# Performance work log

Measured on AMD Instinct MI355X. Metric: run time of the kernel, lower is better.

Reference implementation:

```python
import jax, jax.numpy as jnp
import numpy as np

N = 50000   # nodes
F = 32      # num_node_features
EMB = 32    # embedding_size
R = 8       # num_relations
L = 5       # num_layers
E = 400000  # edges


def setup_inputs() -> dict:
    key = jax.random.key(0)
    ks = jax.random.split(key, 12)
    s = 0.1  # weight scale ~ 1/sqrt(fan_in) for stability over 5 residual layers
    return {
        "x": jax.random.normal(ks[0], (N, F), jnp.float32),
        "edge_index": jax.random.randint(ks[1], (2, E), 0, N, jnp.int32),
        "edge_type": jax.random.randint(ks[2], (E,), 0, R, jnp.int32),
        "edge_dist": jax.random.uniform(ks[3], (E,), jnp.float32),
        "fc_W": jax.random.normal(ks[4], (F, EMB), jnp.float32) * s,
        "fc_b": jnp.zeros((EMB,), jnp.float32),
        "rgcn_W": jax.random.normal(ks[5], (L, R, EMB, EMB), jnp.float32) * s,
        "rgcn_root": jax.random.normal(ks[6], (L, EMB, EMB), jnp.float32) * s,
        "rgcn_bias": jnp.zeros((L, EMB), jnp.float32),
        "mlp_W1": jax.random.normal(ks[7], (1 + R, EMB), jnp.float32) * s,
        "mlp_b1": jnp.zeros((EMB,), jnp.float32),
        "mlp_W2": jax.random.normal(ks[8], (EMB, EMB * EMB), jnp.float32) * s,
        "mlp_b2": jnp.zeros((EMB * EMB,), jnp.float32),
        "nn_root": jax.random.normal(ks[9], (L, EMB, EMB), jnp.float32) * s,
        "nn_bias": jnp.zeros((L, EMB), jnp.float32),
    }


def _forward(x, edge_index, edge_type, edge_dist, fc_W, fc_b, rgcn_W, rgcn_root,
             rgcn_bias, mlp_W1, mlp_b1, mlp_W2, mlp_b2, nn_root, nn_bias):
    n = x.shape[0]
    src, dst = edge_index[0], edge_index[1]  # source_to_target flow

    # edge_attr_c = [distance, onehot(edge_type)] : [E, 1+R]
    onehot = jax.nn.one_hot(edge_type, R, dtype=x.dtype)
    eattr = jnp.concatenate([edge_dist[:, None], onehot], axis=1)

    # Shared edge_mlp -> per-edge [EMB, EMB] weight (same for every NNConv layer)
    We = (jax.nn.relu(eattr @ mlp_W1 + mlp_b1) @ mlp_W2 + mlp_b2).reshape(-1, EMB, EMB)

    # degree for NNConv mean aggregation
    deg = jax.ops.segment_sum(jnp.ones_like(edge_dist), dst, num_segments=n)
    denom = jnp.maximum(deg, 1.0)[:, None]

    # per-relation in-degree for RGCN per-relation mean
    rel_cnt = []
    for r in range(R):
        c = jax.ops.segment_sum((edge_type == r).astype(x.dtype), dst, num_segments=n)
        rel_cnt.append(jnp.maximum(c, 1.0)[:, None])

    h = jax.nn.relu(x @ fc_W + fc_b)
    for l in range(L):
        # RGCNConv: root transform + per-relation mean of W_r x_j
        out = h @ rgcn_root[l] + rgcn_bias[l]
        for r in range(R):
            mask_r = (edge_type == r).astype(h.dtype)[:, None]
            msg = (h @ rgcn_W[l, r])[src] * mask_r  # [E, EMB]
            out = out + jax.ops.segment_sum(msg, dst, num_segments=n) / rel_cnt[r]
        h_disc = jax.nn.relu(out)

        # NNConv: x_j @ Theta(e) per edge, mean-aggregated, + root + bias
        msg = jnp.einsum('ei,eio->eo', h[src], We)  # [E, EMB]
        agg = jax.ops.segment_sum(msg, dst, num_segments=n) / denom
        h_cont = jax.nn.relu(h @ nn_root[l] + agg + nn_bias[l])

        h = h + h_disc + h_cont
    return h


def reference(x, edge_index, edge_type, edge_dist, fc_W, fc_b, rgcn_W, rgcn_root,
              rgcn_bias, mlp_W1, mlp_b1, mlp_W2, mlp_b2, nn_root, nn_bias):
    return _forward(x, edge_index, edge_type, edge_dist, fc_W, fc_b, rgcn_W,
                    rgcn_root, rgcn_bias, mlp_W1, mlp_b1, mlp_W2, mlp_b2,
                    nn_root, nn_bias)
```

## Files before the change

### kernel.cpp

```cpp
#include <hip/hip_runtime.h>

#define N_NODES 50000
#define N_EDGES 400000
#define EMB 32
#define NREL 8
#define NLAYER 5
#define NPB 16
#define NBLK (N_NODES / NPB)
#define KROWS 43
#define NCHUNK 196
#define E2CAP (N_EDGES + 8 * N_NODES)

typedef __attribute__((ext_vector_type(8))) short short8;
typedef __attribute__((ext_vector_type(4))) float f32x4;
typedef __attribute__((ext_vector_type(4))) unsigned int u32x4v;

__device__ __forceinline__ unsigned short f2bf(float f) {
    unsigned u = __float_as_uint(f);
    unsigned r = u + 0x7FFF + ((u >> 16) & 1);
    return (unsigned short)(r >> 16);
}

__device__ __forceinline__ unsigned cvt_pk(float a, float b) {
    unsigned r;
    asm("v_cvt_pk_bf16_f32 %0, %1, %2" : "=v"(r) : "v"(a), "v"(b));
    return r;
}


__global__ __launch_bounds__(256) void fill_kernel(int* __restrict__ zeroblk,
                                                   int2* __restrict__ edge2,
                                                   float* __restrict__ ha,
                                                   float* __restrict__ hb) {
    int i = blockIdx.x * 256 + threadIdx.x;
    if (i < E2CAP) edge2[i] = make_int2(N_NODES, 0);
    if (i < 10 * N_NODES) zeroblk[i] = 0;
    if (i < EMB) { ha[(size_t)N_NODES * EMB + i] = 0.0f; hb[(size_t)N_NODES * EMB + i] = 0.0f; }
}

__global__ __launch_bounds__(256) void hist_kernel(const int* __restrict__ ei,
                                                   const int* __restrict__ et,
                                                   int* __restrict__ deg,
                                                   int* __restrict__ relcnt) {
    int e = blockIdx.x * 256 + threadIdx.x;
    if (e < N_EDGES) {
        int d = ei[N_EDGES + e];
        atomicAdd(&deg[d], 1);
        atomicAdd(&relcnt[d * NREL + et[e]], 1);
    }
}

__device__ __forceinline__ int pdeg_of(int d) {
    return (d > 0 ? d + 7 : 8) & ~7;
}

__global__ __launch_bounds__(256) void nodeprep_kernel(const int* __restrict__ deg,
                                                       const int* __restrict__ relcnt,
                                                       int* __restrict__ bsum,
                                                       float* __restrict__ invdeg,
                                                       float* __restrict__ invcnt,
                                                       unsigned char* __restrict__ perm) {
    __shared__ int wsum[4];
    int tid = threadIdx.x, lane = tid & 63, wv = tid >> 6;
    int i = blockIdx.x * 256 + tid;
    int d = (i < N_NODES) ? deg[i] : 0;
    int v = (i < N_NODES) ? pdeg_of(d) : 0;
    #pragma unroll
    for (int off = 32; off > 0; off >>= 1) v += __shfl_down(v, off, 64);
    if (lane == 0) wsum[wv] = v;
    __syncthreads();
    if (tid == 0) bsum[blockIdx.x] = wsum[0] + wsum[1] + wsum[2] + wsum[3];
    if (i < N_NODES) {
        invdeg[i] = 1.0f / (float)(d > 0 ? d : 1);
        #pragma unroll
        for (int r = 0; r < NREL; r++) {
            int c = relcnt[i * NREL + r];
            invcnt[i * NREL + r] = 1.0f / (float)(c > 0 ? c : 1);
        }
    }
    if (i < NBLK) {
        int dd[NPB]; unsigned char idx[NPB];
        #pragma unroll
        for (int k = 0; k < NPB; k++) { dd[k] = deg[i * NPB + k]; idx[k] = (unsigned char)k; }
        for (int a = 1; a < NPB; a++) {
            int dv = dd[a]; unsigned char iv = idx[a];
            int j = a - 1;
            while (j >= 0 && dd[j] < dv) { dd[j + 1] = dd[j]; idx[j + 1] = idx[j]; j--; }
            dd[j + 1] = dv; idx[j + 1] = iv;
        }
        #pragma unroll
        for (int k = 0; k < NPB; k++) perm[i * NPB + k] = idx[k];
    }
}

__global__ __launch_bounds__(256) void boff_kernel(const int* __restrict__ bsum,
                                                   int* __restrict__ boff,
                                                   int* __restrict__ row_ptr) {
    __shared__ int ws[4];
    int tid = threadIdx.x, lane = tid & 63, w = tid >> 6;
    int v = (tid < NCHUNK) ? bsum[tid] : 0;
    int incl = v;
    #pragma unroll
    for (int off = 1; off < 64; off <<= 1) {
        int t = __shfl_up(incl, off, 64);
        if (lane >= off) incl += t;
    }
    if (lane == 63) ws[w] = incl;
    __syncthreads();
    int add = 0;
    for (int j = 0; j < w; j++) add += ws[j];
    if (tid < NCHUNK) boff[tid] = add + incl - v;
    if (tid == 0) row_ptr[N_NODES] = ws[0] + ws[1] + ws[2] + ws[3];
}

__global__ __launch_bounds__(256) void rptr_kernel(const int* __restrict__ deg,
                                                   const int* __restrict__ boff,
                                                   int* __restrict__ row_ptr) {
    __shared__ int ws[4];
    int tid = threadIdx.x, lane = tid & 63, w = tid >> 6;
    int i = blockIdx.x * 256 + tid;
    int v = (i < N_NODES) ? pdeg_of(deg[i]) : 0;
    int incl = v;
    #pragma unroll
    for (int off = 1; off < 64; off <<= 1) {
        int t = __shfl_up(incl, off, 64);
        if (lane >= off) incl += t;
    }
    if (lane == 63) ws[w] = incl;
    __syncthreads();
    int add = boff[blockIdx.x];
    for (int j = 0; j < w; j++) add += ws[j];
    if (i < N_NODES) row_ptr[i] = add + incl - v;
}

__global__ __launch_bounds__(256) void scatter_kernel(const int* __restrict__ ei,
                                                      const int* __restrict__ et,
                                                      const float* __restrict__ ed,
                                                      const int* __restrict__ row_ptr,
                                                      int* __restrict__ cursor,
                                                      int2* __restrict__ edge2,
                                                      const unsigned char* __restrict__ perm,
                                                      int4* __restrict__ wavetab) {
    int e = blockIdx.x * 256 + threadIdx.x;
    if (e < N_EDGES) {
        int d = ei[N_EDGES + e];
        int pos = row_ptr[d] + atomicAdd(&cursor[d], 1);
        edge2[pos] = make_int2(ei[e] | (et[e] << 16), __float_as_int(ed[e]));
    }
    if (e < NBLK * 8) {
        int b = e >> 3, wv = e & 7;
        int s0 = perm[b * NPB + wv], s1 = perm[b * NPB + (NPB - 1 - wv)];
        int nA = b * NPB + s0, nB = b * NPB + s1;
        int pb0 = row_ptr[nA], pd0 = row_ptr[nA + 1] - pb0;
        int pb1 = row_ptr[nB], pd1 = row_ptr[nB + 1] - pb1;
        wavetab[e] = make_int4(s0 | (s1 << 8), pb0, pb1, pd0 | (pd1 << 16));
    }
}

__global__ __launch_bounds__(256) void wtbf_kernel(const float* __restrict__ W2,
                                                   const float* __restrict__ b2,
                                                   const float* __restrict__ rgcnW,
                                                   const float* __restrict__ rgcnRoot,
                                                   const float* __restrict__ nnRoot,
                                                   unsigned short* __restrict__ WB) {
    int m = blockIdx.x;
    const float* src;
    if (m < 32) src = W2 + (size_t)m * 1024;
    else if (m == 32) src = b2;
    else {
        int t = m - 33, l = t / 10, j = t % 10;
        src = (j < 8) ? rgcnW + (size_t)(l * 8 + j) * 1024
            : (j == 8) ? rgcnRoot + (size_t)l * 1024
                       : nnRoot + (size_t)l * 1024;
    }
    unsigned short* dst = WB + (size_t)m * 1024;
    #pragma unroll
    for (int c = 0; c < 4; c++) {
        int idx = c * 256 + threadIdx.x;
        int o = idx >> 5, k = idx & 31;
        int i = (k >> 1) + ((k & 1) << 4);
        dst[o * 32 + k] = f2bf(src[i * 32 + o]);
    }
}


__global__ __launch_bounds__(256) void fc_kernel(const float* __restrict__ x,
                                                 const float* __restrict__ W,
                                                 const float* __restrict__ b,
                                                 float* __restrict__ h) {
    __shared__ __align__(16) float xt[8][EMB];
    int tid = threadIdx.x;
    int nl = tid >> 5, lane = tid & 31;
    int n0 = blockIdx.x * 8;
    xt[tid >> 5][tid & 31] = x[n0 * EMB + tid];
    __syncthreads();
    float acc = b[lane];
    #pragma unroll
    for (int i = 0; i < EMB; i++) acc += xt[nl][i] * W[i * EMB + lane];
    int ol = ((lane & 15) << 1) | (lane >> 4);
    h[(n0 + nl) * EMB + ol] = fmaxf(acc, 0.0f);
}


__device__ __forceinline__ void gath(const float* __restrict__ h, int4 E, int m,
                                     float2& ga, float2& gb) {
    ga = *(const float2*)&h[((E.x & 0xFFFF) << 5) + 2 * m];
    gb = *(const float2*)&h[((E.z & 0xFFFF) << 5) + 2 * m];
}

__device__ __forceinline__ void proc_pair(int4 E, float2 ga, float2 gb,
                                          const float2* wrb2f, float w10_0, float w10_1,
                                          unsigned selm, int m,
                                          unsigned& A0s, unsigned& A1s, unsigned& ASs,
                                          unsigned& B0s, unsigned& B1s) {
    int ra = (E.x >> 16) & 7, rb = (E.z >> 16) & 7;
    float2 wa = wrb2f[ra * 16 + m];
    float2 wb = wrb2f[rb * 16 + m];
    float da = __int_as_float(E.y), db = __int_as_float(E.w);
    float hA0 = fmaxf(fmaf(da, w10_0, wa.x), 0.f);
    float hA1 = fmaxf(fmaf(da, w10_1, wa.y), 0.f);
    float hB0 = fmaxf(fmaf(db, w10_0, wb.x), 0.f);
    float hB1 = fmaxf(fmaf(db, w10_1, wb.y), 0.f);
    A0s = cvt_pk(hA0, hB0);
    A1s = cvt_pk(hA1, hB1);
    ASs = cvt_pk((float)((selm >> ra) & 1u), (float)((selm >> rb) & 1u));
    B0s = cvt_pk(ga.x, gb.x);
    B1s = cvt_pk(ga.y, gb.y);
}

__device__ __forceinline__ void mfma6(const unsigned* fa0v, const unsigned* fa1v,
                                      const unsigned* fasv, const unsigned* fb0v,
                                      const unsigned* fb1v,
                                      f32x4& aP00, f32x4& aP01, f32x4& aP10, f32x4& aP11,
                                      f32x4& aS0, f32x4& aS1) {
    u32x4v u0 = {fa0v[0], fa0v[1], fa0v[2], fa0v[3]};
    u32x4v u1 = {fa1v[0], fa1v[1], fa1v[2], fa1v[3]};
    u32x4v us = {fasv[0], fasv[1], fasv[2], fasv[3]};
    u32x4v v0 = {fb0v[0], fb0v[1], fb0v[2], fb0v[3]};
    u32x4v v1 = {fb1v[0], fb1v[1], fb1v[2], fb1v[3]};
    short8 A0 = __builtin_bit_cast(short8, u0);
    short8 A1 = __builtin_bit_cast(short8, u1);
    short8 AS = __builtin_bit_cast(short8, us);
    short8 B0 = __builtin_bit_cast(short8, v0);
    short8 B1 = __builtin_bit_cast(short8, v1);
    aP00 = __builtin_amdgcn_mfma_f32_16x16x32_bf16(A0, B0, aP00, 0, 0, 0);
    aP01 = __builtin_amdgcn_mfma_f32_16x16x32_bf16(A0, B1, aP01, 0, 0, 0);
    aP10 = __builtin_amdgcn_mfma_f32_16x16x32_bf16(A1, B0, aP10, 0, 0, 0);
    aP11 = __builtin_amdgcn_mfma_f32_16x16x32_bf16(A1, B1, aP11, 0, 0, 0);
    aS0  = __builtin_amdgcn_mfma_f32_16x16x32_bf16(AS, B0, aS0, 0, 0, 0);
    aS1  = __builtin_amdgcn_mfma_f32_16x16x32_bf16(AS, B1, aS1, 0, 0, 0);
}

__device__ __forceinline__ void edge_pass(const float* __restrict__ h,
                                          const int2* __restrict__ edge2,
                                          const float2* wrb2f,
                                          int pb, int pe, int quad, int m,
                                          float w10_0, float w10_1, unsigned selm,
                                          int4 E0, float2 g0a, float2 g0b,
                                          f32x4& aP00, f32x4& aP01, f32x4& aP10,
                                          f32x4& aP11, f32x4& aS0, f32x4& aS1) {
    {
        unsigned fa0v[4] = {0,0,0,0}, fa1v[4] = {0,0,0,0}, fasv[4] = {0,0,0,0};
        unsigned fb0v[4] = {0,0,0,0}, fb1v[4] = {0,0,0,0};
        proc_pair(E0, g0a, g0b, wrb2f, w10_0, w10_1, selm, m,
                  fa0v[0], fa1v[0], fasv[0], fb0v[0], fb1v[0]);
        if (pb + 8 < pe) {
            int4 E = *(const int4*)&edge2[pb + 8 + quad * 2];
            float2 ga, gb; gath(h, E, m, ga, gb);
            proc_pair(E, ga, gb, wrb2f, w10_0, w10_1, selm, m,
                      fa0v[1], fa1v[1], fasv[1], fb0v[1], fb1v[1]);
        }
        if (pb + 16 < pe) {
            int4 E = *(const int4*)&edge2[pb + 16 + quad * 2];
            float2 ga, gb; gath(h, E, m, ga, gb);
            proc_pair(E, ga, gb, wrb2f, w10_0, w10_1, selm, m,
                      fa0v[2], fa1v[2], fasv[2], fb0v[2], fb1v[2]);
        }
        if (pb + 24 < pe) {
            int4 E = *(const int4*)&edge2[pb + 24 + quad * 2];
            float2 ga, gb; gath(h, E, m, ga, gb);
            proc_pair(E, ga, gb, wrb2f, w10_0, w10_1, selm, m,
                      fa0v[3], fa1v[3], fasv[3], fb0v[3], fb1v[3]);
        }
        mfma6(fa0v, fa1v, fasv, fb0v, fb1v, aP00, aP01, aP10, aP11, aS0, aS1);
    }
    for (int c0 = pb + 32; c0 < pe; c0 += 32) {
        unsigned fa0v[4] = {0,0,0,0}, fa1v[4] = {0,0,0,0}, fasv[4] = {0,0,0,0};
        unsigned fb0v[4] = {0,0,0,0}, fb1v[4] = {0,0,0,0};
        {
            int4 E = *(const int4*)&edge2[c0 + quad * 2];
            float2 ga, gb; gath(h, E, m, ga, gb);
            proc_pair(E, ga, gb, wrb2f, w10_0, w10_1, selm, m,
                      fa0v[0], fa1v[0], fasv[0], fb0v[0], fb1v[0]);
        }
        if (c0 + 8 < pe) {
            int4 E = *(const int4*)&edge2[c0 + 8 + quad * 2];
            float2 ga, gb; gath(h, E, m, ga, gb);
            proc_pair(E, ga, gb, wrb2f, w10_0, w10_1, selm, m,
                      fa0v[1], fa1v[1], fasv[1], fb0v[1], fb1v[1]);
        }
        if (c0 + 16 < pe) {
            int4 E = *(const int4*)&edge2[c0 + 16 + quad * 2];
            float2 ga, gb; gath(h, E, m, ga, gb);
            proc_pair(E, ga, gb, wrb2f, w10_0, w10_1, selm, m,
                      fa0v[2], fa1v[2], fasv[2], fb0v[2], fb1v[2]);
        }
        if (c0 + 24 < pe) {
            int4 E = *(const int4*)&edge2[c0 + 24 + quad * 2];
            float2 ga, gb; gath(h, E, m, ga, gb);
            proc_pair(E, ga, gb, wrb2f, w10_0, w10_1, selm, m,
                      fa0v[3], fa1v[3], fasv[3], fb0v[3], fb1v[3]);
        }
        mfma6(fa0v, fa1v, fasv, fb0v, fb1v, aP00, aP01, aP10, aP11, aS0, aS1);
    }
}

__device__ __forceinline__ void stage_node(unsigned short (*P)[EMB], int quad, int m,
                                           float idg, const float* __restrict__ invcnt_n,
                                           const float* __restrict__ hrow,
                                           const f32x4& aP00, const f32x4& aP01,
                                           const f32x4& aP10, const f32x4& aP11,
                                           const f32x4& aS0, const f32x4& aS1) {
    #pragma unroll
    for (int reg = 0; reg < 4; ++reg) {
        const int row = quad * 4 + reg;
        *(unsigned*)&P[row][2 * m]      = cvt_pk(aP00[reg] * idg, aP01[reg] * idg);
        *(unsigned*)&P[row + 16][2 * m] = cvt_pk(aP10[reg] * idg, aP11[reg] * idg);
        if (row <= 8) {
            const float sc = (row == 0) ? idg : invcnt_n[row - 1];
            *(unsigned*)&P[32 + row][2 * m] = cvt_pk(aS0[reg] * sc, aS1[reg] * sc);
        }
    }
    if (quad < 2) {
        float2 hh = *(const float2*)&hrow[2 * m];
        *(unsigned*)&P[41 + quad][2 * m] = cvt_pk(hh.x, hh.y);
    }
}

__global__ __launch_bounds__(512, 6) void layer_kernel(
    const float* __restrict__ h,
    const int2* __restrict__ edge2,
    const int4* __restrict__ wavetab,
    const float* __restrict__ invdeg,
    const float* __restrict__ invcnt,
    const float* __restrict__ W1,
    const float* __restrict__ b1,
    const unsigned short* __restrict__ WBs,
    const unsigned short* __restrict__ WBl,
    const float* __restrict__ rgcnBias_l,
    const float* __restrict__ nnBias_l,
    float* __restrict__ hout,
    int last)
{
    __shared__ __align__(16) unsigned short P_lds[NPB][KROWS][EMB];
    __shared__ __align__(16) float2 wrb2f[NREL * 16];

    const int tid = threadIdx.x;
    const int n0 = blockIdx.x * NPB;

    if (tid < 128) {
        int r = tid >> 4, mi = tid & 15;
        wrb2f[r * 16 + mi] = make_float2(W1[(1 + r) * EMB + mi] + b1[mi],
                                         W1[(1 + r) * EMB + mi + 16] + b1[mi + 16]);
    }

    const int l    = tid & 63;
    const int w    = tid >> 6;
    const int quad = l >> 4;
    const int m    = l & 15;
    const float w10_0 = W1[m];
    const float w10_1 = W1[m + 16];
    const unsigned selm = (m == 0) ? 0xFFu : (m <= 8 ? (1u << (m - 1)) : 0u);

    int4 wt = wavetab[blockIdx.x * 8 + w];
    const int hw0 = wt.x & 0xFF, hw1 = (wt.x >> 8) & 0xFF;
    const int pb0 = wt.y, pe0 = wt.y + (wt.w & 0xFFFF);
    const int pb1 = wt.z, pe1 = wt.z + (int)((unsigned)wt.w >> 16);
    int4 E0 = *(const int4*)&edge2[pb0 + quad * 2];
    int4 E1 = *(const int4*)&edge2[pb1 + quad * 2];
    float2 g0a, g0b, g1a, g1b;
    gath(h, E0, m, g0a, g0b);
    gath(h, E1, m, g1a, g1b);

    __syncthreads();

    {
        f32x4 aP00 = {0,0,0,0}, aP01 = {0,0,0,0}, aP10 = {0,0,0,0}, aP11 = {0,0,0,0};
        f32x4 aS0 = {0,0,0,0}, aS1 = {0,0,0,0};
        edge_pass(h, edge2, wrb2f, pb0, pe0, quad, m, w10_0, w10_1, selm,
                  E0, g0a, g0b, aP00, aP01, aP10, aP11, aS0, aS1);
        const int n = n0 + hw0;
        stage_node(P_lds[hw0], quad, m, invdeg[n], invcnt + (size_t)n * NREL,
                   h + (size_t)n * EMB, aP00, aP01, aP10, aP11, aS0, aS1);
    }
    {
        f32x4 aP00 = {0,0,0,0}, aP01 = {0,0,0,0}, aP10 = {0,0,0,0}, aP11 = {0,0,0,0};
        f32x4 aS0 = {0,0,0,0}, aS1 = {0,0,0,0};
        edge_pass(h, edge2, wrb2f, pb1, pe1, quad, m, w10_0, w10_1, selm,
                  E1, g1a, g1b, aP00, aP01, aP10, aP11, aS0, aS1);
        const int n = n0 + hw1;
        stage_node(P_lds[hw1], quad, m, invdeg[n], invcnt + (size_t)n * NREL,
                   h + (size_t)n * EMB, aP00, aP01, aP10, aP11, aS0, aS1);
    }
    __syncthreads();

    const int node16 = l & 15;
    const int o0 = l & 15;

    f32x4 accN0 = {0,0,0,0}, accN1 = {0,0,0,0};
    f32x4 accR0 = {0,0,0,0}, accR1 = {0,0,0,0};

    #pragma unroll
    for (int j = 0; j < 6; j++) {
        const int rr = w + 8 * j;
        if (rr < KROWS) {
            const unsigned short* Bsrc = (rr < 33) ? (WBs + (size_t)rr * 1024)
                                                   : (WBl + (size_t)(rr - 33) * 1024);
            short8 bf0 = *(const short8*)(Bsrc + o0 * 32 + quad * 8);
            short8 bf1 = *(const short8*)(Bsrc + (o0 + 16) * 32 + quad * 8);
            short8 a = *(const short8*)&P_lds[node16][rr][quad * 8];
            if (rr <= 32 || rr == 42) {
                accN0 = __builtin_amdgcn_mfma_f32_16x16x32_bf16(a, bf0, accN0, 0, 0, 0);
                accN1 = __builtin_amdgcn_mfma_f32_16x16x32_bf16(a, bf1, accN1, 0, 0, 0);
            } else {
                accR0 = __builtin_amdgcn_mfma_f32_16x16x32_bf16(a, bf0, accR0, 0, 0, 0);
                accR1 = __builtin_amdgcn_mfma_f32_16x16x32_bf16(a, bf1, accR1, 0, 0, 0);
            }
        }
    }
    __syncthreads();

    float* RedAll = (float*)&P_lds[0][0][0];
    {
        float* my = RedAll + w * 1024;
        #pragma unroll
        for (int reg = 0; reg < 4; reg++) {
            int nd = quad * 4 + reg;
            my[nd * 32 + o0]            = accN0[reg];
            my[nd * 32 + o0 + 16]       = accN1[reg];
            my[512 + nd * 32 + o0]      = accR0[reg];
            my[512 + nd * 32 + o0 + 16] = accR1[reg];
        }
    }
    __syncthreads();

    {
        const int hw2 = tid >> 5, lane = tid & 31;
        const int n2 = n0 + hw2;
        float sn = 0.0f, sr = 0.0f;
        #pragma unroll
        for (int ww = 0; ww < 8; ww++) {
            sn += RedAll[ww * 1024 + tid];
            sr += RedAll[ww * 1024 + 512 + tid];
        }
        const int il = ((lane & 15) << 1) | (lane >> 4);
        float hd = h[(size_t)n2 * EMB + il];
        float o_r = fmaxf(sr + rgcnBias_l[lane], 0.0f);
        float o_n = fmaxf(sn + nnBias_l[lane], 0.0f);
        hout[(size_t)n2 * EMB + (last ? lane : il)] = hd + o_r + o_n;
    }
}


extern "C" void kernel_launch(void* const* d_in, const int* in_sizes, int n_in,
                              void* d_out, int out_size, void* d_ws, size_t ws_size,
                              hipStream_t stream) {
    const float* x        = (const float*)d_in[0];
    const int*   ei       = (const int*)d_in[1];
    const int*   et       = (const int*)d_in[2];
    const float* ed       = (const float*)d_in[3];
    const float* fcW      = (const float*)d_in[4];
    const float* fcb      = (const float*)d_in[5];
    const float* rgcnW    = (const float*)d_in[6];
    const float* rgcnRoot = (const float*)d_in[7];
    const float* rgcnBias = (const float*)d_in[8];
    const float* W1       = (const float*)d_in[9];
    const float* b1       = (const float*)d_in[10];
    const float* W2       = (const float*)d_in[11];
    const float* b2       = (const float*)d_in[12];
    const float* nnRoot   = (const float*)d_in[13];
    const float* nnBias   = (const float*)d_in[14];

    float* ws = (float*)d_ws;
    float* h_a    = ws;  ws += (size_t)(N_NODES + 1) * EMB;
    float* h_b    = ws;  ws += (size_t)(N_NODES + 1) * EMB;
    float* invdeg = ws;  ws += (size_t)N_NODES;
    float* invcnt = ws;  ws += (size_t)N_NODES * NREL;
    unsigned short* WB = (unsigned short*)ws;  ws += (size_t)83 * 1024 / 2;
    int2* edge2   = (int2*)ws;     ws += (size_t)E2CAP * 2;
    int* row_ptr  = (int*)ws;      ws += (size_t)(N_NODES + 1);
    int* bsum     = (int*)ws;      ws += (size_t)NCHUNK;
    int* boff     = (int*)ws;      ws += (size_t)NCHUNK;
    int* deg      = (int*)ws;      ws += (size_t)N_NODES;
    int* relcnt   = (int*)ws;      ws += (size_t)N_NODES * NREL;
    int* cursor   = (int*)ws;      ws += (size_t)N_NODES;
    unsigned char* perm = (unsigned char*)ws;  ws += (size_t)NBLK * NPB / 4;
    int4* wavetab = (int4*)ws;     ws += (size_t)NBLK * 8 * 4;
    (void)in_sizes; (void)n_in; (void)out_size; (void)ws_size;

    fill_kernel<<<(E2CAP + 255) / 256, 256, 0, stream>>>(deg, edge2, h_a, h_b);
    hist_kernel<<<(N_EDGES + 255) / 256, 256, 0, stream>>>(ei, et, deg, relcnt);
    nodeprep_kernel<<<NCHUNK, 256, 0, stream>>>(deg, relcnt, bsum, invdeg, invcnt, perm);
    boff_kernel<<<1, 256, 0, stream>>>(bsum, boff, row_ptr);
    rptr_kernel<<<NCHUNK, 256, 0, stream>>>(deg, boff, row_ptr);
    scatter_kernel<<<(N_EDGES + 255) / 256, 256, 0, stream>>>(ei, et, ed, row_ptr,
                                                              cursor, edge2, perm, wavetab);
    wtbf_kernel<<<83, 256, 0, stream>>>(W2, b2, rgcnW, rgcnRoot, nnRoot, WB);
    fc_kernel<<<N_NODES / 8, 256, 0, stream>>>(x, fcW, fcb, h_a);

    const float* hin = h_a;
    float* houtb = h_b;
    for (int l = 0; l < NLAYER; l++) {
        float* dst = (l == NLAYER - 1) ? (float*)d_out : houtb;
        layer_kernel<<<NBLK, 512, 0, stream>>>(
            hin, edge2, wavetab, invdeg, invcnt, W1, b1,
            WB, WB + (size_t)(33 + l * 10) * 1024,
            rgcnBias + (size_t)l * EMB,
            nnBias + (size_t)l * EMB,
            dst, (l == NLAYER - 1) ? 1 : 0);
        float* old_in = (float*)hin;
        hin = dst;
        houtb = old_in;
    }
}
```

Baseline: 395.8 us.

## Schedule nodes globally by padded degree bucket, one node per wave

Replaces the per-block sort of 16 consecutive nodes with a global counting sort of nodes into padded-degree buckets. Each 1024-thread block now handles 16 nodes of similar degree, one node per wave, so waves inside a block stay balanced. The output reduction becomes two-phase across 16 waves, and the edge-list padding is written only into the padding slots inside scatter instead of a full prefill. The trade-offs are global atomics on 32 bucket counters, scattered node access per block that loses locality, and larger blocks that may lower occupancy.

```diff
diff --git a/kernel.cpp b/kernel.cpp
--- a/kernel.cpp
+++ b/kernel.cpp
@@ -27,14 +27,16 @@
     return r;
 }
 
+__device__ __forceinline__ int pdeg_of(int d) {
+    return (d > 0 ? d + 7 : 8) & ~7;
+}
+
 
 __global__ __launch_bounds__(256) void fill_kernel(int* __restrict__ zeroblk,
-                                                   int2* __restrict__ edge2,
                                                    float* __restrict__ ha,
                                                    float* __restrict__ hb) {
     int i = blockIdx.x * 256 + threadIdx.x;
-    if (i < E2CAP) edge2[i] = make_int2(N_NODES, 0);
-    if (i < 10 * N_NODES) zeroblk[i] = 0;
+    if (i < 10 * N_NODES + 64) zeroblk[i] = 0;
     if (i < EMB) { ha[(size_t)N_NODES * EMB + i] = 0.0f; hb[(size_t)N_NODES * EMB + i] = 0.0f; }
 }
 
@@ -50,16 +52,12 @@
     }
 }
 
-__device__ __forceinline__ int pdeg_of(int d) {
-    return (d > 0 ? d + 7 : 8) & ~7;
-}
-
 __global__ __launch_bounds__(256) void nodeprep_kernel(const int* __restrict__ deg,
                                                        const int* __restrict__ relcnt,
                                                        int* __restrict__ bsum,
                                                        float* __restrict__ invdeg,
                                                        float* __restrict__ invcnt,
-                                                       unsigned char* __restrict__ perm) {
+                                                       int* __restrict__ bcnt) {
     __shared__ int wsum[4];
     int tid = threadIdx.x, lane = tid & 63, wv = tid >> 6;
     int i = blockIdx.x * 256 + tid;
@@ -77,25 +75,16 @@
             int c = relcnt[i * NREL + r];
             invcnt[i * NREL + r] = 1.0f / (float)(c > 0 ? c : 1);
         }
-    }
-    if (i < NBLK) {
-        int dd[NPB]; unsigned char idx[NPB];
-        #pragma unroll
-        for (int k = 0; k < NPB; k++) { dd[k] = deg[i * NPB + k]; idx[k] = (unsigned char)k; }
-        for (int a = 1; a < NPB; a++) {
-            int dv = dd[a]; unsigned char iv = idx[a];
-            int j = a - 1;
-            while (j >= 0 && dd[j] < dv) { dd[j + 1] = dd[j]; idx[j + 1] = idx[j]; j--; }
-            dd[j + 1] = dv; idx[j + 1] = iv;
-        }
-        #pragma unroll
-        for (int k = 0; k < NPB; k++) perm[i * NPB + k] = idx[k];
+        int bkt = pdeg_of(d) >> 3; bkt = (bkt > 32 ? 32 : bkt) - 1;
+        atomicAdd(&bcnt[bkt], 1);
     }
 }
 
 __global__ __launch_bounds__(256) void boff_kernel(const int* __restrict__ bsum,
                                                    int* __restrict__ boff,
-                                                   int* __restrict__ row_ptr) {
+                                                   int* __restrict__ row_ptr,
+                                                   const int* __restrict__ bcnt,
+                                                   int* __restrict__ bcur) {
     __shared__ int ws[4];
     int tid = threadIdx.x, lane = tid & 63, w = tid >> 6;
     int v = (tid < NCHUNK) ? bsum[tid] : 0;
@@ -110,16 +99,23 @@
     int add = 0;
     for (int j = 0; j < w; j++) add += ws[j];
     if (tid < NCHUNK) boff[tid] = add + incl - v;
-    if (tid == 0) row_ptr[N_NODES] = ws[0] + ws[1] + ws[2] + ws[3];
+    if (tid == 0) {
+        row_ptr[N_NODES] = ws[0] + ws[1] + ws[2] + ws[3];
+        int acc = 0;
+        for (int b = 0; b < 32; b++) { bcur[b] = acc; acc += bcnt[b]; }
+    }
 }
 
 __global__ __launch_bounds__(256) void rptr_kernel(const int* __restrict__ deg,
                                                    const int* __restrict__ boff,
-                                                   int* __restrict__ row_ptr) {
+                                                   int* __restrict__ row_ptr,
+                                                   int* __restrict__ bcur,
+                                                   int* __restrict__ sched) {
     __shared__ int ws[4];
     int tid = threadIdx.x, lane = tid & 63, w = tid >> 6;
     int i = blockIdx.x * 256 + tid;
-    int v = (i < N_NODES) ? pdeg_of(deg[i]) : 0;
+    int d = (i < N_NODES) ? deg[i] : 0;
+    int v = (i < N_NODES) ? pdeg_of(d) : 0;
     int incl = v;
     #pragma unroll
     for (int off = 1; off < 64; off <<= 1) {
@@ -130,16 +126,22 @@
     __syncthreads();
     int add = boff[blockIdx.x];
     for (int j = 0; j < w; j++) add += ws[j];
-    if (i < N_NODES) row_ptr[i] = add + incl - v;
+    if (i < N_NODES) {
+        row_ptr[i] = add + incl - v;
+        int bkt = pdeg_of(d) >> 3; bkt = (bkt > 32 ? 32 : bkt) - 1;
+        int pos = atomicAdd(&bcur[bkt], 1);
+        sched[pos] = i;
+    }
 }
 
 __global__ __launch_bounds__(256) void scatter_kernel(const int* __restrict__ ei,
                                                       const int* __restrict__ et,
                                                       const float* __restrict__ ed,
                                                       const int* __restrict__ row_ptr,
+                                                      const int* __restrict__ deg,
                                                       int* __restrict__ cursor,
                                                       int2* __restrict__ edge2,
-                                                      const unsigned char* __restrict__ perm,
+                                                      const int* __restrict__ sched,
                                                       int4* __restrict__ wavetab) {
     int e = blockIdx.x * 256 + threadIdx.x;
     if (e < N_EDGES) {
@@ -147,13 +149,12 @@
         int pos = row_ptr[d] + atomicAdd(&cursor[d], 1);
         edge2[pos] = make_int2(ei[e] | (et[e] << 16), __float_as_int(ed[e]));
     }
-    if (e < NBLK * 8) {
-        int b = e >> 3, wv = e & 7;
-        int s0 = perm[b * NPB + wv], s1 = perm[b * NPB + (NPB - 1 - wv)];
-        int nA = b * NPB + s0, nB = b * NPB + s1;
-        int pb0 = row_ptr[nA], pd0 = row_ptr[nA + 1] - pb0;
-        int pb1 = row_ptr[nB], pd1 = row_ptr[nB + 1] - pb1;
-        wavetab[e] = make_int4(s0 | (s1 << 8), pb0, pb1, pd0 | (pd1 << 16));
+    if (e < N_NODES) {
+        int base = row_ptr[e], d = deg[e], pd = pdeg_of(d);
+        for (int p = base + d; p < base + pd; ++p)
+            edge2[p] = make_int2(N_NODES, 0);
+        int node = sched[e];
+        wavetab[e] = make_int4(node, row_ptr[node], pdeg_of(deg[node]), 0);
     }
 }
 
@@ -287,29 +288,14 @@
     for (int c0 = pb + 32; c0 < pe; c0 += 32) {
         unsigned fa0v[4] = {0,0,0,0}, fa1v[4] = {0,0,0,0}, fasv[4] = {0,0,0,0};
         unsigned fb0v[4] = {0,0,0,0}, fb1v[4] = {0,0,0,0};
-        {
-            int4 E = *(const int4*)&edge2[c0 + quad * 2];
-            float2 ga, gb; gath(h, E, m, ga, gb);
-            proc_pair(E, ga, gb, wrb2f, w10_0, w10_1, selm, m,
-                      fa0v[0], fa1v[0], fasv[0], fb0v[0], fb1v[0]);
-        }
-        if (c0 + 8 < pe) {
-            int4 E = *(const int4*)&edge2[c0 + 8 + quad * 2];
-            float2 ga, gb; gath(h, E, m, ga, gb);
-            proc_pair(E, ga, gb, wrb2f, w10_0, w10_1, selm, m,
-                      fa0v[1], fa1v[1], fasv[1], fb0v[1], fb1v[1]);
-        }
-        if (c0 + 16 < pe) {
-            int4 E = *(const int4*)&edge2[c0 + 16 + quad * 2];
-            float2 ga, gb; gath(h, E, m, ga, gb);
-            proc_pair(E, ga, gb, wrb2f, w10_0, w10_1, selm, m,
-                      fa0v[2], fa1v[2], fasv[2], fb0v[2], fb1v[2]);
-        }
-        if (c0 + 24 < pe) {
-            int4 E = *(const int4*)&edge2[c0 + 24 + quad * 2];
-            float2 ga, gb; gath(h, E, m, ga, gb);
-            proc_pair(E, ga, gb, wrb2f, w10_0, w10_1, selm, m,
-                      fa0v[3], fa1v[3], fasv[3], fb0v[3], fb1v[3]);
+        #pragma unroll
+        for (int jp = 0; jp < 4; ++jp) {
+            if (c0 + jp * 8 < pe) {
+                int4 E = *(const int4*)&edge2[c0 + jp * 8 + quad * 2];
+                float2 ga, gb; gath(h, E, m, ga, gb);
+                proc_pair(E, ga, gb, wrb2f, w10_0, w10_1, selm, m,
+                          fa0v[jp], fa1v[jp], fasv[jp], fb0v[jp], fb1v[jp]);
+            }
         }
         mfma6(fa0v, fa1v, fasv, fb0v, fb1v, aP00, aP01, aP10, aP11, aS0, aS1);
     }
@@ -337,7 +323,7 @@
     }
 }
 
-__global__ __launch_bounds__(512, 6) void layer_kernel(
+__global__ __launch_bounds__(1024, 8) void layer_kernel(
     const float* __restrict__ h,
     const int2* __restrict__ edge2,
     const int4* __restrict__ wavetab,
@@ -354,9 +340,9 @@
 {
     __shared__ __align__(16) unsigned short P_lds[NPB][KROWS][EMB];
     __shared__ __align__(16) float2 wrb2f[NREL * 16];
+    __shared__ int nodeid[NPB];
 
     const int tid = threadIdx.x;
-    const int n0 = blockIdx.x * NPB;
 
     if (tid < 128) {
         int r = tid >> 4, mi = tid & 15;
@@ -372,35 +358,22 @@
     const float w10_1 = W1[m + 16];
     const unsigned selm = (m == 0) ? 0xFFu : (m <= 8 ? (1u << (m - 1)) : 0u);
 
-    int4 wt = wavetab[blockIdx.x * 8 + w];
-    const int hw0 = wt.x & 0xFF, hw1 = (wt.x >> 8) & 0xFF;
-    const int pb0 = wt.y, pe0 = wt.y + (wt.w & 0xFFFF);
-    const int pb1 = wt.z, pe1 = wt.z + (int)((unsigned)wt.w >> 16);
-    int4 E0 = *(const int4*)&edge2[pb0 + quad * 2];
-    int4 E1 = *(const int4*)&edge2[pb1 + quad * 2];
-    float2 g0a, g0b, g1a, g1b;
+    int4 wt = wavetab[blockIdx.x * NPB + w];
+    const int node = wt.x, pb = wt.y, pe = wt.y + wt.z;
+    if (l == 0) nodeid[w] = node;
+    int4 E0 = *(const int4*)&edge2[pb + quad * 2];
+    float2 g0a, g0b;
     gath(h, E0, m, g0a, g0b);
-    gath(h, E1, m, g1a, g1b);
 
     __syncthreads();
 
     {
         f32x4 aP00 = {0,0,0,0}, aP01 = {0,0,0,0}, aP10 = {0,0,0,0}, aP11 = {0,0,0,0};
         f32x4 aS0 = {0,0,0,0}, aS1 = {0,0,0,0};
-        edge_pass(h, edge2, wrb2f, pb0, pe0, quad, m, w10_0, w10_1, selm,
+        edge_pass(h, edge2, wrb2f, pb, pe, quad, m, w10_0, w10_1, selm,
                   E0, g0a, g0b, aP00, aP01, aP10, aP11, aS0, aS1);
-        const int n = n0 + hw0;
-        stage_node(P_lds[hw0], quad, m, invdeg[n], invcnt + (size_t)n * NREL,
-                   h + (size_t)n * EMB, aP00, aP01, aP10, aP11, aS0, aS1);
-    }
-    {
-        f32x4 aP00 = {0,0,0,0}, aP01 = {0,0,0,0}, aP10 = {0,0,0,0}, aP11 = {0,0,0,0};
-        f32x4 aS0 = {0,0,0,0}, aS1 = {0,0,0,0};
-        edge_pass(h, edge2, wrb2f, pb1, pe1, quad, m, w10_0, w10_1, selm,
-                  E1, g1a, g1b, aP00, aP01, aP10, aP11, aS0, aS1);
-        const int n = n0 + hw1;
-        stage_node(P_lds[hw1], quad, m, invdeg[n], invcnt + (size_t)n * NREL,
-                   h + (size_t)n * EMB, aP00, aP01, aP10, aP11, aS0, aS1);
+        stage_node(P_lds[w], quad, m, invdeg[node], invcnt + (size_t)node * NREL,
+                   h + (size_t)node * EMB, aP00, aP01, aP10, aP11, aS0, aS1);
     }
     __syncthreads();
 
@@ -411,8 +384,8 @@
     f32x4 accR0 = {0,0,0,0}, accR1 = {0,0,0,0};
 
     #pragma unroll
-    for (int j = 0; j < 6; j++) {
-        const int rr = w + 8 * j;
+    for (int j = 0; j < 3; j++) {
+        const int rr = w + 16 * j;
         if (rr < KROWS) {
             const unsigned short* Bsrc = (rr < 33) ? (WBs + (size_t)rr * 1024)
                                                    : (WBl + (size_t)(rr - 33) * 1024);
@@ -431,7 +404,7 @@
     __syncthreads();
 
     float* RedAll = (float*)&P_lds[0][0][0];
-    {
+    if (w < 8) {
         float* my = RedAll + w * 1024;
         #pragma unroll
         for (int reg = 0; reg < 4; reg++) {
@@ -443,10 +416,22 @@
         }
     }
     __syncthreads();
-
-    {
+    if (w >= 8) {
+        float* my = RedAll + (w - 8) * 1024;
+        #pragma unroll
+        for (int reg = 0; reg < 4; reg++) {
+            int nd = quad * 4 + reg;
+            my[nd * 32 + o0]            += accN0[reg];
+            my[nd * 32 + o0 + 16]       += accN1[reg];
+            my[512 + nd * 32 + o0]      += accR0[reg];
+            my[512 + nd * 32 + o0 + 16] += accR1[reg];
+        }
+    }
+    __syncthreads();
+
+    if (tid < 512) {
         const int hw2 = tid >> 5, lane = tid & 31;
-        const int n2 = n0 + hw2;
+        const int n2 = nodeid[hw2];
         float sn = 0.0f, sr = 0.0f;
         #pragma unroll
         for (int ww = 0; ww < 8; ww++) {
@@ -494,17 +479,19 @@
     int* deg      = (int*)ws;      ws += (size_t)N_NODES;
     int* relcnt   = (int*)ws;      ws += (size_t)N_NODES * NREL;
     int* cursor   = (int*)ws;      ws += (size_t)N_NODES;
-    unsigned char* perm = (unsigned char*)ws;  ws += (size_t)NBLK * NPB / 4;
-    int4* wavetab = (int4*)ws;     ws += (size_t)NBLK * 8 * 4;
+    int* bcnt     = (int*)ws;      ws += 32;
+    int* bcur     = (int*)ws;      ws += 32;
+    int* sched    = (int*)ws;      ws += (size_t)N_NODES;
+    int4* wavetab = (int4*)ws;     ws += (size_t)N_NODES * 4;
     (void)in_sizes; (void)n_in; (void)out_size; (void)ws_size;
 
-    fill_kernel<<<(E2CAP + 255) / 256, 256, 0, stream>>>(deg, edge2, h_a, h_b);
+    fill_kernel<<<(10 * N_NODES + 64 + 255) / 256, 256, 0, stream>>>(deg, h_a, h_b);
     hist_kernel<<<(N_EDGES + 255) / 256, 256, 0, stream>>>(ei, et, deg, relcnt);
-    nodeprep_kernel<<<NCHUNK, 256, 0, stream>>>(deg, relcnt, bsum, invdeg, invcnt, perm);
-    boff_kernel<<<1, 256, 0, stream>>>(bsum, boff, row_ptr);
-    rptr_kernel<<<NCHUNK, 256, 0, stream>>>(deg, boff, row_ptr);
-    scatter_kernel<<<(N_EDGES + 255) / 256, 256, 0, stream>>>(ei, et, ed, row_ptr,
-                                                              cursor, edge2, perm, wavetab);
+    nodeprep_kernel<<<NCHUNK, 256, 0, stream>>>(deg, relcnt, bsum, invdeg, invcnt, bcnt);
+    boff_kernel<<<1, 256, 0, stream>>>(bsum, boff, row_ptr, bcnt, bcur);
+    rptr_kernel<<<NCHUNK, 256, 0, stream>>>(deg, boff, row_ptr, bcur, sched);
+    scatter_kernel<<<(N_EDGES + 255) / 256, 256, 0, stream>>>(ei, et, ed, row_ptr, deg,
+                                                              cursor, edge2, sched, wavetab);
     wtbf_kernel<<<83, 256, 0, stream>>>(W2, b2, rgcnW, rgcnRoot, nnRoot, WB);
     fc_kernel<<<N_NODES / 8, 256, 0, stream>>>(x, fcW, fcb, h_a);
 
@@ -512,7 +499,7 @@
     float* houtb = h_b;
     for (int l = 0; l < NLAYER; l++) {
         float* dst = (l == NLAYER - 1) ? (float*)d_out : houtb;
-        layer_kernel<<<NBLK, 512, 0, stream>>>(
+        layer_kernel<<<NBLK, 1024, 0, stream>>>(
             hin, edge2, wavetab, invdeg, invcnt, W1, b1,
             WB, WB + (size_t)(33 + l * 10) * 1024,
             rgcnBias + (size_t)l * EMB,
```

Measured after the change: 1.252 ms. +216.3%, slower.

## Keep a bf16 shadow copy of node features for edge gathers

Applied to the files above, without the earlier changes.

Each layer and the fc kernel now write a packed bf16 copy of the node features alongside the fp32 copy. The edge gathers and root-row staging read this bf16 array, which halves the bytes of the random neighbor gathers and removes per-edge fp32-to-bf16 conversion. Separately, padding slots in edge2 are filled only where needed in the scatter kernel instead of the whole buffer being initialised in fill_kernel. The cost is an extra bf16 write per layer and more workspace.

```diff
diff --git a/kernel.cpp b/kernel.cpp
--- a/kernel.cpp
+++ b/kernel.cpp
@@ -27,15 +27,23 @@
     return r;
 }
 
+__device__ __forceinline__ int pdeg_of(int d) {
+    return (d > 0 ? d + 7 : 8) & ~7;
+}
+
 
 __global__ __launch_bounds__(256) void fill_kernel(int* __restrict__ zeroblk,
-                                                   int2* __restrict__ edge2,
                                                    float* __restrict__ ha,
-                                                   float* __restrict__ hb) {
+                                                   float* __restrict__ hb,
+                                                   unsigned* __restrict__ hb16a,
+                                                   unsigned* __restrict__ hb16b) {
     int i = blockIdx.x * 256 + threadIdx.x;
-    if (i < E2CAP) edge2[i] = make_int2(N_NODES, 0);
     if (i < 10 * N_NODES) zeroblk[i] = 0;
     if (i < EMB) { ha[(size_t)N_NODES * EMB + i] = 0.0f; hb[(size_t)N_NODES * EMB + i] = 0.0f; }
+    if (i < EMB / 2) {
+        hb16a[(size_t)N_NODES * (EMB / 2) + i] = 0u;
+        hb16b[(size_t)N_NODES * (EMB / 2) + i] = 0u;
+    }
 }
 
 __global__ __launch_bounds__(256) void hist_kernel(const int* __restrict__ ei,
@@ -48,10 +56,6 @@
         atomicAdd(&deg[d], 1);
         atomicAdd(&relcnt[d * NREL + et[e]], 1);
     }
-}
-
-__device__ __forceinline__ int pdeg_of(int d) {
-    return (d > 0 ? d + 7 : 8) & ~7;
 }
 
 __global__ __launch_bounds__(256) void nodeprep_kernel(const int* __restrict__ deg,
@@ -137,6 +141,7 @@
                                                       const int* __restrict__ et,
                                                       const float* __restrict__ ed,
                                                       const int* __restrict__ row_ptr,
+                                                      const int* __restrict__ deg,
                                                       int* __restrict__ cursor,
                                                       int2* __restrict__ edge2,
                                                       const unsigned char* __restrict__ perm,
@@ -146,6 +151,11 @@
         int d = ei[N_EDGES + e];
         int pos = row_ptr[d] + atomicAdd(&cursor[d], 1);
         edge2[pos] = make_int2(ei[e] | (et[e] << 16), __float_as_int(ed[e]));
+    }
+    if (e < N_NODES) {
+        int base = row_ptr[e], d = deg[e], pd = pdeg_of(d);
+        for (int p = base + d; p < base + pd; ++p)
+            edge2[p] = make_int2(N_NODES, 0);
     }
     if (e < NBLK * 8) {
         int b = e >> 3, wv = e & 7;
@@ -187,7 +197,8 @@
 __global__ __launch_bounds__(256) void fc_kernel(const float* __restrict__ x,
                                                  const float* __restrict__ W,
                                                  const float* __restrict__ b,
-                                                 float* __restrict__ h) {
+                                                 float* __restrict__ h,
+                                                 unsigned short* __restrict__ hb16) {
     __shared__ __align__(16) float xt[8][EMB];
     int tid = threadIdx.x;
     int nl = tid >> 5, lane = tid & 31;
@@ -197,18 +208,23 @@
     float acc = b[lane];
     #pragma unroll
     for (int i = 0; i < EMB; i++) acc += xt[nl][i] * W[i * EMB + lane];
+    float v = fmaxf(acc, 0.0f);
     int ol = ((lane & 15) << 1) | (lane >> 4);
-    h[(n0 + nl) * EMB + ol] = fmaxf(acc, 0.0f);
-}
-
-
-__device__ __forceinline__ void gath(const float* __restrict__ h, int4 E, int m,
-                                     float2& ga, float2& gb) {
-    ga = *(const float2*)&h[((E.x & 0xFFFF) << 5) + 2 * m];
-    gb = *(const float2*)&h[((E.z & 0xFFFF) << 5) + 2 * m];
-}
-
-__device__ __forceinline__ void proc_pair(int4 E, float2 ga, float2 gb,
+    h[(size_t)(n0 + nl) * EMB + ol] = v;
+    float pv = __shfl_down(v, 16, 32);
+    unsigned pk = cvt_pk(v, pv);
+    if (lane < 16)
+        *(unsigned*)&hb16[(size_t)(n0 + nl) * EMB + 2 * lane] = pk;
+}
+
+
+__device__ __forceinline__ void gath(const unsigned short* __restrict__ hb16, int4 E, int m,
+                                     unsigned& uA, unsigned& uB) {
+    uA = *(const unsigned*)(hb16 + (((size_t)(E.x & 0xFFFF)) << 5) + 2 * m);
+    uB = *(const unsigned*)(hb16 + (((size_t)(E.z & 0xFFFF)) << 5) + 2 * m);
+}
+
+__device__ __forceinline__ void proc_pair(int4 E, unsigned uA, unsigned uB,
                                           const float2* wrb2f, float w10_0, float w10_1,
                                           unsigned selm, int m,
                                           unsigned& A0s, unsigned& A1s, unsigned& ASs,
@@ -224,8 +240,8 @@
     A0s = cvt_pk(hA0, hB0);
     A1s = cvt_pk(hA1, hB1);
     ASs = cvt_pk((float)((selm >> ra) & 1u), (float)((selm >> rb) & 1u));
-    B0s = cvt_pk(ga.x, gb.x);
-    B1s = cvt_pk(ga.y, gb.y);
+    B0s = (uA & 0xFFFFu) | (uB << 16);
+    B1s = (uA >> 16) | (uB & 0xFFFF0000u);
 }
 
 __device__ __forceinline__ void mfma6(const unsigned* fa0v, const unsigned* fa1v,
@@ -251,35 +267,35 @@
     aS1  = __builtin_amdgcn_mfma_f32_16x16x32_bf16(AS, B1, aS1, 0, 0, 0);
 }
 
-__device__ __forceinline__ void edge_pass(const float* __restrict__ h,
+__device__ __forceinline__ void edge_pass(const unsigned short* __restrict__ hb16,
                                           const int2* __restrict__ edge2,
                                           const float2* wrb2f,
                                           int pb, int pe, int quad, int m,
                                           float w10_0, float w10_1, unsigned selm,
-                                          int4 E0, float2 g0a, float2 g0b,
+                                          int4 E0, unsigned u0A, unsigned u0B,
                                           f32x4& aP00, f32x4& aP01, f32x4& aP10,
                                           f32x4& aP11, f32x4& aS0, f32x4& aS1) {
     {
         unsigned fa0v[4] = {0,0,0,0}, fa1v[4] = {0,0,0,0}, fasv[4] = {0,0,0,0};
         unsigned fb0v[4] = {0,0,0,0}, fb1v[4] = {0,0,0,0};
-        proc_pair(E0, g0a, g0b, wrb2f, w10_0, w10_1, selm, m,
+        proc_pair(E0, u0A, u0B, wrb2f, w10_0, w10_1, selm, m,
                   fa0v[0], fa1v[0], fasv[0], fb0v[0], fb1v[0]);
         if (pb + 8 < pe) {
             int4 E = *(const int4*)&edge2[pb + 8 + quad * 2];
-            float2 ga, gb; gath(h, E, m, ga, gb);
-            proc_pair(E, ga, gb, wrb2f, w10_0, w10_1, selm, m,
+            unsigned uA, uB; gath(hb16, E, m, uA, uB);
+            proc_pair(E, uA, uB, wrb2f, w10_0, w10_1, selm, m,
                       fa0v[1], fa1v[1], fasv[1], fb0v[1], fb1v[1]);
         }
         if (pb + 16 < pe) {
             int4 E = *(const int4*)&edge2[pb + 16 + quad * 2];
-            float2 ga, gb; gath(h, E, m, ga, gb);
-            proc_pair(E, ga, gb, wrb2f, w10_0, w10_1, selm, m,
+            unsigned uA, uB; gath(hb16, E, m, uA, uB);
+            proc_pair(E, uA, uB, wrb2f, w10_0, w10_1, selm, m,
                       fa0v[2], fa1v[2], fasv[2], fb0v[2], fb1v[2]);
         }
         if (pb + 24 < pe) {
             int4 E = *(const int4*)&edge2[pb + 24 + quad * 2];
-            float2 ga, gb; gath(h, E, m, ga, gb);
-            proc_pair(E, ga, gb, wrb2f, w10_0, w10_1, selm, m,
+            unsigned uA, uB; gath(hb16, E, m, uA, uB);
+            proc_pair(E, uA, uB, wrb2f, w10_0, w10_1, selm, m,
                       fa0v[3], fa1v[3], fasv[3], fb0v[3], fb1v[3]);
         }
         mfma6(fa0v, fa1v, fasv, fb0v, fb1v, aP00, aP01, aP10, aP11, aS0, aS1);
@@ -287,58 +303,44 @@
     for (int c0 = pb + 32; c0 < pe; c0 += 32) {
         unsigned fa0v[4] = {0,0,0,0}, fa1v[4] = {0,0,0,0}, fasv[4] = {0,0,0,0};
         unsigned fb0v[4] = {0,0,0,0}, fb1v[4] = {0,0,0,0};
-        {
-            int4 E = *(const int4*)&edge2[c0 + quad * 2];
-            float2 ga, gb; gath(h, E, m, ga, gb);
-            proc_pair(E, ga, gb, wrb2f, w10_0, w10_1, selm, m,
-                      fa0v[0], fa1v[0], fasv[0], fb0v[0], fb1v[0]);
-        }
-        if (c0 + 8 < pe) {
-            int4 E = *(const int4*)&edge2[c0 + 8 + quad * 2];
-            float2 ga, gb; gath(h, E, m, ga, gb);
-            proc_pair(E, ga, gb, wrb2f, w10_0, w10_1, selm, m,
-                      fa0v[1], fa1v[1], fasv[1], fb0v[1], fb1v[1]);
-        }
-        if (c0 + 16 < pe) {
-            int4 E = *(const int4*)&edge2[c0 + 16 + quad * 2];
-            float2 ga, gb; gath(h, E, m, ga, gb);
-            proc_pair(E, ga, gb, wrb2f, w10_0, w10_1, selm, m,
-                      fa0v[2], fa1v[2], fasv[2], fb0v[2], fb1v[2]);
-        }
-        if (c0 + 24 < pe) {
-            int4 E = *(const int4*)&edge2[c0 + 24 + quad * 2];
-            float2 ga, gb; gath(h, E, m, ga, gb);
-            proc_pair(E, ga, gb, wrb2f, w10_0, w10_1, selm, m,
-                      fa0v[3], fa1v[3], fasv[3], fb0v[3], fb1v[3]);
+        #pragma unroll
+        for (int jp = 0; jp < 4; ++jp) {
+            if (c0 + jp * 8 < pe) {
+                int4 E = *(const int4*)&edge2[c0 + jp * 8 + quad * 2];
+                unsigned uA, uB; gath(hb16, E, m, uA, uB);
+                proc_pair(E, uA, uB, wrb2f, w10_0, w10_1, selm, m,
+                          fa0v[jp], fa1v[jp], fasv[jp], fb0v[jp], fb1v[jp]);
+            }
         }
         mfma6(fa0v, fa1v, fasv, fb0v, fb1v, aP00, aP01, aP10, aP11, aS0, aS1);
     }
 }
 
-__device__ __forceinline__ void stage_node(unsigned short (*P)[EMB], int quad, int m,
+__device__ __forceinline__ void stage_node(unsigned short* __restrict__ P, int quad, int m,
                                            float idg, const float* __restrict__ invcnt_n,
-                                           const float* __restrict__ hrow,
+                                           const unsigned short* __restrict__ hb16row,
                                            const f32x4& aP00, const f32x4& aP01,
                                            const f32x4& aP10, const f32x4& aP11,
                                            const f32x4& aS0, const f32x4& aS1) {
     #pragma unroll
     for (int reg = 0; reg < 4; ++reg) {
         const int row = quad * 4 + reg;
-        *(unsigned*)&P[row][2 * m]      = cvt_pk(aP00[reg] * idg, aP01[reg] * idg);
-        *(unsigned*)&P[row + 16][2 * m] = cvt_pk(aP10[reg] * idg, aP11[reg] * idg);
+        *(unsigned*)&P[row * EMB + 2 * m]        = cvt_pk(aP00[reg] * idg, aP01[reg] * idg);
+        *(unsigned*)&P[(row + 16) * EMB + 2 * m] = cvt_pk(aP10[reg] * idg, aP11[reg] * idg);
         if (row <= 8) {
             const float sc = (row == 0) ? idg : invcnt_n[row - 1];
-            *(unsigned*)&P[32 + row][2 * m] = cvt_pk(aS0[reg] * sc, aS1[reg] * sc);
+            *(unsigned*)&P[(32 + row) * EMB + 2 * m] = cvt_pk(aS0[reg] * sc, aS1[reg] * sc);
         }
     }
     if (quad < 2) {
-        float2 hh = *(const float2*)&hrow[2 * m];
-        *(unsigned*)&P[41 + quad][2 * m] = cvt_pk(hh.x, hh.y);
+        unsigned hh = *(const unsigned*)(hb16row + 2 * m);
+        *(unsigned*)&P[(41 + quad) * EMB + 2 * m] = hh;
     }
 }
 
 __global__ __launch_bounds__(512, 6) void layer_kernel(
     const float* __restrict__ h,
+    const unsigned short* __restrict__ hb16,
     const int2* __restrict__ edge2,
     const int4* __restrict__ wavetab,
     const float* __restrict__ invdeg,
@@ -350,9 +352,10 @@
     const float* __restrict__ rgcnBias_l,
     const float* __restrict__ nnBias_l,
     float* __restrict__ hout,
+    unsigned short* __restrict__ hb16out,
     int last)
 {
-    __shared__ __align__(16) unsigned short P_lds[NPB][KROWS][EMB];
+    __shared__ __align__(16) unsigned short P_lds[NPB * KROWS * EMB];
     __shared__ __align__(16) float2 wrb2f[NREL * 16];
 
     const int tid = threadIdx.x;
@@ -378,29 +381,31 @@
     const int pb1 = wt.z, pe1 = wt.z + (int)((unsigned)wt.w >> 16);
     int4 E0 = *(const int4*)&edge2[pb0 + quad * 2];
     int4 E1 = *(const int4*)&edge2[pb1 + quad * 2];
-    float2 g0a, g0b, g1a, g1b;
-    gath(h, E0, m, g0a, g0b);
-    gath(h, E1, m, g1a, g1b);
+    unsigned u0A, u0B, u1A, u1B;
+    gath(hb16, E0, m, u0A, u0B);
+    gath(hb16, E1, m, u1A, u1B);
 
     __syncthreads();
 
     {
         f32x4 aP00 = {0,0,0,0}, aP01 = {0,0,0,0}, aP10 = {0,0,0,0}, aP11 = {0,0,0,0};
         f32x4 aS0 = {0,0,0,0}, aS1 = {0,0,0,0};
-        edge_pass(h, edge2, wrb2f, pb0, pe0, quad, m, w10_0, w10_1, selm,
-                  E0, g0a, g0b, aP00, aP01, aP10, aP11, aS0, aS1);
+        edge_pass(hb16, edge2, wrb2f, pb0, pe0, quad, m, w10_0, w10_1, selm,
+                  E0, u0A, u0B, aP00, aP01, aP10, aP11, aS0, aS1);
         const int n = n0 + hw0;
-        stage_node(P_lds[hw0], quad, m, invdeg[n], invcnt + (size_t)n * NREL,
-                   h + (size_t)n * EMB, aP00, aP01, aP10, aP11, aS0, aS1);
+        stage_node(P_lds + (size_t)hw0 * KROWS * EMB, quad, m, invdeg[n],
+                   invcnt + (size_t)n * NREL, hb16 + (size_t)n * EMB,
+                   aP00, aP01, aP10, aP11, aS0, aS1);
     }
     {
         f32x4 aP00 = {0,0,0,0}, aP01 = {0,0,0,0}, aP10 = {0,0,0,0}, aP11 = {0,0,0,0};
         f32x4 aS0 = {0,0,0,0}, aS1 = {0,0,0,0};
-        edge_pass(h, edge2, wrb2f, pb1, pe1, quad, m, w10_0, w10_1, selm,
-                  E1, g1a, g1b, aP00, aP01, aP10, aP11, aS0, aS1);
+        edge_pass(hb16, edge2, wrb2f, pb1, pe1, quad, m, w10_0, w10_1, selm,
+                  E1, u1A, u1B, aP00, aP01, aP10, aP11, aS0, aS1);
         const int n = n0 + hw1;
-        stage_node(P_lds[hw1], quad, m, invdeg[n], invcnt + (size_t)n * NREL,
-                   h + (size_t)n * EMB, aP00, aP01, aP10, aP11, aS0, aS1);
+        stage_node(P_lds + (size_t)hw1 * KROWS * EMB, quad, m, invdeg[n],
+                   invcnt + (size_t)n * NREL, hb16 + (size_t)n * EMB,
+                   aP00, aP01, aP10, aP11, aS0, aS1);
     }
     __syncthreads();
 
@@ -418,7 +423,7 @@
                                                    : (WBl + (size_t)(rr - 33) * 1024);
             short8 bf0 = *(const short8*)(Bsrc + o0 * 32 + quad * 8);
             short8 bf1 = *(const short8*)(Bsrc + (o0 + 16) * 32 + quad * 8);
-            short8 a = *(const short8*)&P_lds[node16][rr][quad * 8];
+            short8 a = *(const short8*)&P_lds[(size_t)node16 * KROWS * EMB + rr * EMB + quad * 8];
             if (rr <= 32 || rr == 42) {
                 accN0 = __builtin_amdgcn_mfma_f32_16x16x32_bf16(a, bf0, accN0, 0, 0, 0);
                 accN1 = __builtin_amdgcn_mfma_f32_16x16x32_bf16(a, bf1, accN1, 0, 0, 0);
@@ -430,7 +435,7 @@
     }
     __syncthreads();
 
-    float* RedAll = (float*)&P_lds[0][0][0];
+    float* RedAll = (float*)&P_lds[0];
     {
         float* my = RedAll + w * 1024;
         #pragma unroll
@@ -457,7 +462,14 @@
         float hd = h[(size_t)n2 * EMB + il];
         float o_r = fmaxf(sr + rgcnBias_l[lane], 0.0f);
         float o_n = fmaxf(sn + nnBias_l[lane], 0.0f);
-        hout[(size_t)n2 * EMB + (last ? lane : il)] = hd + o_r + o_n;
+        float outv = hd + o_r + o_n;
+        hout[(size_t)n2 * EMB + (last ? lane : il)] = outv;
+        if (!last) {
+            float pv = __shfl_down(outv, 16, 32);
+            unsigned pk = cvt_pk(outv, pv);
+            if (lane < 16)
+                *(unsigned*)&hb16out[(size_t)n2 * EMB + 2 * lane] = pk;
+        }
     }
 }
 
@@ -484,6 +496,8 @@
     float* ws = (float*)d_ws;
     float* h_a    = ws;  ws += (size_t)(N_NODES + 1) * EMB;
     float* h_b    = ws;  ws += (size_t)(N_NODES + 1) * EMB;
+    unsigned short* hb16_a = (unsigned short*)ws;  ws += (size_t)(N_NODES + 1) * EMB / 2;
+    unsigned short* hb16_b = (unsigned short*)ws;  ws += (size_t)(N_NODES + 1) * EMB / 2;
     float* invdeg = ws;  ws += (size_t)N_NODES;
     float* invcnt = ws;  ws += (size_t)N_NODES * NREL;
     unsigned short* WB = (unsigned short*)ws;  ws += (size_t)83 * 1024 / 2;
@@ -494,32 +508,38 @@
     int* deg      = (int*)ws;      ws += (size_t)N_NODES;
     int* relcnt   = (int*)ws;      ws += (size_t)N_NODES * NREL;
     int* cursor   = (int*)ws;      ws += (size_t)N_NODES;
-    unsigned char* perm = (unsigned char*)ws;  ws += (size_t)NBLK * NPB / 4;
+    unsigned char* perm = (unsigned char*)ws;  ws += (size_t)(NBLK * NPB + 3) / 4;
     int4* wavetab = (int4*)ws;     ws += (size_t)NBLK * 8 * 4;
     (void)in_sizes; (void)n_in; (void)out_size; (void)ws_size;
 
-    fill_kernel<<<(E2CAP + 255) / 256, 256, 0, stream>>>(deg, edge2, h_a, h_b);
+    fill_kernel<<<(10 * N_NODES + 255) / 256, 256, 0, stream>>>(deg, h_a, h_b,
+                                                                (unsigned*)hb16_a,
+                                                                (unsigned*)hb16_b);
     hist_kernel<<<(N_EDGES + 255) / 256, 256, 0, stream>>>(ei, et, deg, relcnt);
     nodeprep_kernel<<<NCHUNK, 256, 0, stream>>>(deg, relcnt, bsum, invdeg, invcnt, perm);
     boff_kernel<<<1, 256, 0, stream>>>(bsum, boff, row_ptr);
     rptr_kernel<<<NCHUNK, 256, 0, stream>>>(deg, boff, row_ptr);
-    scatter_kernel<<<(N_EDGES + 255) / 256, 256, 0, stream>>>(ei, et, ed, row_ptr,
+    scatter_kernel<<<(N_EDGES + 255) / 256, 256, 0, stream>>>(ei, et, ed, row_ptr, deg,
                                                               cursor, edge2, perm, wavetab);
     wtbf_kernel<<<83, 256, 0, stream>>>(W2, b2, rgcnW, rgcnRoot, nnRoot, WB);
-    fc_kernel<<<N_NODES / 8, 256, 0, stream>>>(x, fcW, fcb, h_a);
+    fc_kernel<<<N_NODES / 8, 256, 0, stream>>>(x, fcW, fcb, h_a, hb16_a);
 
     const float* hin = h_a;
+    const unsigned short* hbin = hb16_a;
     float* houtb = h_b;
+    unsigned short* hboutb = hb16_b;
     for (int l = 0; l < NLAYER; l++) {
-        float* dst = (l == NLAYER - 1) ? (float*)d_out : houtb;
+        int last = (l == NLAYER - 1) ? 1 : 0;
+        float* dst = last ? (float*)d_out : houtb;
         layer_kernel<<<NBLK, 512, 0, stream>>>(
-            hin, edge2, wavetab, invdeg, invcnt, W1, b1,
+            hin, hbin, edge2, wavetab, invdeg, invcnt, W1, b1,
             WB, WB + (size_t)(33 + l * 10) * 1024,
             rgcnBias + (size_t)l * EMB,
             nnBias + (size_t)l * EMB,
-            dst, (l == NLAYER - 1) ? 1 : 0);
+            dst, hboutb, last);
         float* old_in = (float*)hin;
-        hin = dst;
-        houtb = old_in;
-    }
-}
+        unsigned short* old_hb = (unsigned short*)hbin;
+        hin = dst; hbin = hboutb;
+        houtb = old_in; hboutb = old_hb;
+    }
+}
```

Result: faster. 382.5 us (-3.4%).
